# Kernel optimization log

Hardware: AMD Instinct MI355X
Metric: run time of the kernel (lower is better)

## Reference

```python
import jax, jax.numpy as jnp
import numpy as np

E = 23   # unique experts
K = 3    # active experts per token

def setup_inputs() -> dict:
    key = jax.random.key(0)
    ks = jax.random.split(key, 11)
    d, h, B, N = 1024, 768, 16, 196
    s = 0.02  # init scale so sigmoid gate is non-saturated
    return {
        "x":      jax.random.normal(ks[0], (B, N, d), jnp.float32),
        "gate_w": jax.random.normal(ks[1], (d, E), jnp.float32) * s,
        "gate_b": jnp.zeros((E,), jnp.float32),
        "w1":     jax.random.normal(ks[2], (E, d, h), jnp.float32) * s,
        "b1":     jnp.zeros((E, h), jnp.float32),
        "w2":     jax.random.normal(ks[3], (E, h, d), jnp.float32) * s,
        "b2":     jnp.zeros((E, d), jnp.float32),
        "ws1":    jax.random.normal(ks[4], (d, h), jnp.float32) * s,
        "bs1":    jnp.zeros((h,), jnp.float32),
        "ws2":    jax.random.normal(ks[5], (h, d), jnp.float32) * s,
        "bs2":    jnp.zeros((d,), jnp.float32),
    }

def reference(x, gate_w, gate_b, w1, b1, w2, b2, ws1, bs1, ws2, bs2):
    o_shape = x.shape
    xt = x.reshape(-1, o_shape[-1])            # [T, d]
    T = xt.shape[0]

    # gating: sigmoid gate, top-3 (the 'bias' buffer in the source is zeros)
    gw = jax.nn.sigmoid(xt @ gate_w + gate_b)  # [T, E]
    top_vals, top_idx = jax.lax.top_k(gw, K)   # [T, K]
    tw = top_vals / top_vals.sum(-1, keepdims=True)

    # dense combine weights: tw scattered to [T, E] (0 for unselected experts)
    w_dense = jnp.zeros_like(gw).at[jnp.arange(T)[:, None], top_idx].add(tw)

    # expert MLPs (dense-masked equivalent of the grouped dispatch)
    hh = jax.nn.gelu(jnp.einsum('td,edh->teh', xt, w1) + b1, approximate=False)
    eo = jnp.einsum('teh,ehd->ted', hh, w2) + b2          # [T, E, d]

    # shared expert
    shared = jax.nn.gelu(xt @ ws1 + bs1, approximate=False) @ ws2 + bs2

    out = shared + jnp.einsum('ted,te->td', eo, w_dense)  # [T, d]

    # aux load-balancing loss
    gwn = gw / gw.sum(-1, keepdims=True)
    P = gwn.mean(0)                                       # [E]
    counts = jnp.zeros((E,), gw.dtype).at[top_idx.reshape(-1)].add(1.0)
    Fv = E * counts / (K * T)
    aux = (P * Fv).sum()

    return out.reshape(o_shape), aux
```

## Files before the change

### kernel.cpp

```cpp
#include <hip/hip_runtime.h>
#include <hip/hip_bf16.h>

#define T_TOK 3136
#define DDIM  1024
#define HDIM  768
#define NEXP  23
#define TOPK  3
#define MTILE 128
#define NTILE 128
#define KTILE 32
#define LDSP  40
#define MAX_TILES_PER_E 25
#define MAX_SLOTS 16384
#define GATE_BLOCKS 1568
#define NBLK_T 13

typedef __attribute__((ext_vector_type(8))) short  short8;
typedef __attribute__((ext_vector_type(4))) short  short4v;
typedef __attribute__((ext_vector_type(2))) short  short2v;
typedef __attribute__((ext_vector_type(4))) float  floatx4;

__device__ __forceinline__ short f2b(float f) {
    union { float f; unsigned u; } v; v.f = f;
    unsigned r = v.u + 0x7FFFu + ((v.u >> 16) & 1u);
    return (short)(r >> 16);
}
__device__ __forceinline__ float b2f(short s) {
    union { unsigned u; float f; } v; v.u = ((unsigned)(unsigned short)s) << 16; return v.f;
}
__device__ __forceinline__ float gelu_exact(float v) {
    return 0.5f * v * (1.0f + erff(v * 0.70710678118654752f));
}

__global__ __launch_bounds__(256) void gwt_kernel(const float* __restrict__ gw, float* __restrict__ gwT) {
    __shared__ float tile[32][33];
    const int kt = blockIdx.x;
    const int tx = threadIdx.x & 31, ty = threadIdx.x >> 5;
    #pragma unroll
    for (int i = 0; i < 4; i++) {
        int k = ty + i * 8;
        tile[k][tx] = (tx < NEXP) ? gw[(size_t)(kt * 32 + k) * NEXP + tx] : 0.f;
    }
    __syncthreads();
    #pragma unroll
    for (int i = 0; i < 4; i++) {
        int e = ty + i * 8;
        if (e < 24) gwT[(size_t)e * DDIM + kt * 32 + tx] = tile[tx][e];
    }
}

__global__ __launch_bounds__(256) void prep_w_kernel(
    const float* __restrict__ w1, const float* __restrict__ ws1,
    const float* __restrict__ w2, const float* __restrict__ ws2,
    short* __restrict__ w1t, short* __restrict__ ws1t,
    short* __restrict__ w2t, short* __restrict__ ws2t)
{
    const int z = blockIdx.z;
    const float* src; short* dst; int SK, SN;
    if (z < NEXP + 1) {
        src = (z < NEXP) ? w1 + (size_t)z * DDIM * HDIM : ws1;
        dst = (z < NEXP) ? w1t + (size_t)z * DDIM * HDIM : ws1t;
        SK = DDIM; SN = HDIM;
    } else {
        int e = z - (NEXP + 1);
        src = (e < NEXP) ? w2 + (size_t)e * DDIM * HDIM : ws2;
        dst = (e < NEXP) ? w2t + (size_t)e * DDIM * HDIM : ws2t;
        SK = HDIM; SN = DDIM;
    }
    const int nt = blockIdx.x, kt = blockIdx.y;
    if (nt * 32 >= SN || kt * 64 >= SK) return;
    __shared__ float tile[64][33];
    const int tx = threadIdx.x & 31, ty = threadIdx.x >> 5;
    #pragma unroll
    for (int i = 0; i < 8; i++)
        tile[ty + i * 8][tx] = src[(size_t)(kt * 64 + ty + i * 8) * SN + nt * 32 + tx];
    __syncthreads();
    #pragma unroll
    for (int i = 0; i < 4; i++) {
        int n = ty + i * 8;
        short2v sv = { f2b(tile[2 * tx][n]), f2b(tile[2 * tx + 1][n]) };
        *(short2v*)&dst[(size_t)(nt * 32 + n) * SK + kt * 64 + 2 * tx] = sv;
    }
}

__global__ __launch_bounds__(256) void xcvt_kernel(const float* __restrict__ x, short* __restrict__ xb) {
    int i = blockIdx.x * 256 + threadIdx.x;
    float4 v = ((const float4*)x)[i];
    short4v s = { f2b(v.x), f2b(v.y), f2b(v.z), f2b(v.w) };
    ((short4v*)xb)[i] = s;
}

__global__ __launch_bounds__(256) void gate_kernel(
    const float* __restrict__ x, const float* __restrict__ gwT, const float* __restrict__ gb,
    float* __restrict__ gwn, int* __restrict__ top_idx, float* __restrict__ top_w)
{
    const int tid = threadIdx.x;
    const int lane = tid & 63, wave = tid >> 6;
    const int ebase = wave * 6;
    __shared__ float sg[24];

    for (int t = blockIdx.x; t < T_TOK; t += GATE_BLOCKS) {
        const float4* xr4 = (const float4*)(x + (size_t)t * DDIM);
        float4 xv[4];
        #pragma unroll
        for (int j = 0; j < 4; j++) xv[j] = xr4[j * 64 + lane];

        double a0 = 0, a1 = 0, a2 = 0, a3 = 0, a4 = 0, a5 = 0;
        #pragma unroll
        for (int j = 0; j < 4; j++) {
            const float4* gp = (const float4*)gwT + (size_t)ebase * 256 + j * 64 + lane;
            float4 g0 = gp[0 * 256], g1 = gp[1 * 256], g2 = gp[2 * 256];
            float4 g3 = gp[3 * 256], g4 = gp[4 * 256], g5 = gp[5 * 256];
            float4 xj = xv[j];
            a0 += (double)xj.x * g0.x + (double)xj.y * g0.y + (double)xj.z * g0.z + (double)xj.w * g0.w;
            a1 += (double)xj.x * g1.x + (double)xj.y * g1.y + (double)xj.z * g1.z + (double)xj.w * g1.w;
            a2 += (double)xj.x * g2.x + (double)xj.y * g2.y + (double)xj.z * g2.z + (double)xj.w * g2.w;
            a3 += (double)xj.x * g3.x + (double)xj.y * g3.y + (double)xj.z * g3.z + (double)xj.w * g3.w;
            a4 += (double)xj.x * g4.x + (double)xj.y * g4.y + (double)xj.z * g4.z + (double)xj.w * g4.w;
            a5 += (double)xj.x * g5.x + (double)xj.y * g5.y + (double)xj.z * g5.z + (double)xj.w * g5.w;
        }
        #pragma unroll
        for (int off = 32; off > 0; off >>= 1) {
            a0 += __shfl_xor(a0, off);
            a1 += __shfl_xor(a1, off);
            a2 += __shfl_xor(a2, off);
            a3 += __shfl_xor(a3, off);
            a4 += __shfl_xor(a4, off);
            a5 += __shfl_xor(a5, off);
        }

        if (lane == 0) {
            double av[6] = { a0, a1, a2, a3, a4, a5 };
            #pragma unroll
            for (int i = 0; i < 6; i++) {
                int e = ebase + i;
                if (e < NEXP) {
                    float z = (float)av[i] + gb[e];
                    sg[e] = 1.0f / (1.0f + expf(-z));
                }
            }
        }
        __syncthreads();

        if (tid < NEXP) {
            float s = 0.f;
            #pragma unroll
            for (int e = 0; e < NEXP; e++) s += sg[e];
            gwn[(size_t)t * NEXP + tid] = sg[tid] / s;
        }
        if (tid == 0) {
            float v0 = -1.f, v1 = -1.f, v2 = -1.f; int i0 = 0, i1 = 0, i2 = 0;
            for (int e = 0; e < NEXP; e++) {
                float v = sg[e];
                if (v > v0)      { v2 = v1; i2 = i1; v1 = v0; i1 = i0; v0 = v; i0 = e; }
                else if (v > v1) { v2 = v1; i2 = i1; v1 = v; i1 = e; }
                else if (v > v2) { v2 = v; i2 = e; }
            }
            float ts = v0 + v1 + v2;
            top_idx[t * 3 + 0] = i0; top_w[t * 3 + 0] = v0 / ts;
            top_idx[t * 3 + 1] = i1; top_w[t * 3 + 1] = v1 / ts;
            top_idx[t * 3 + 2] = i2; top_w[t * 3 + 2] = v2 / ts;
        }
        __syncthreads();
    }
}

__global__ __launch_bounds__(256) void hist_kernel(
    const int* __restrict__ top_idx, int* __restrict__ block_hist, int* __restrict__ counts)
{
    __shared__ int h[NEXP];
    const int b = blockIdx.x, tid = threadIdx.x;
    if (tid < NEXP) h[tid] = 0;
    __syncthreads();
    int t = b * 256 + tid;
    if (t < T_TOK) {
        atomicAdd(&h[top_idx[t * 3 + 0]], 1);
        atomicAdd(&h[top_idx[t * 3 + 1]], 1);
        atomicAdd(&h[top_idx[t * 3 + 2]], 1);
    }
    __syncthreads();
    if (tid < NEXP) {
        block_hist[b * NEXP + tid] = h[tid];
        atomicAdd(&counts[tid], h[tid]);
    }
}

__global__ __launch_bounds__(256) void offsets_kernel(
    const int* __restrict__ counts, const int* __restrict__ block_hist,
    int* __restrict__ offs, int* __restrict__ ntl, int* __restrict__ block_base,
    int* __restrict__ slot_t)
{
    __shared__ int soffs[NEXP + 1];
    if (threadIdx.x == 0) {
        int o = 0;
        for (int e = 0; e < NEXP; e++) {
            int nt = (counts[e] + MTILE - 1) / MTILE;
            ntl[e] = nt; offs[e] = o; soffs[e] = o; o += nt * MTILE;
        }
        ntl[NEXP] = (T_TOK + MTILE - 1) / MTILE;
        offs[NEXP] = o; soffs[NEXP] = o; o += ntl[NEXP] * MTILE;
        offs[NEXP + 1] = o;
    }
    __syncthreads();
    if (threadIdx.x < NEXP) {
        int e = threadIdx.x;
        int run = soffs[e];
        for (int b = 0; b < NBLK_T; b++) {
            block_base[b * NEXP + e] = run;
            run += block_hist[b * NEXP + e];
        }
    }
    for (int i = threadIdx.x; i < MAX_SLOTS; i += 256) slot_t[i] = 0;
}

__global__ __launch_bounds__(256) void scatter_kernel(
    const int* __restrict__ top_idx, const int* __restrict__ offs,
    const int* __restrict__ block_base,
    int* __restrict__ slot_t, int* __restrict__ slot_of)
{
    __shared__ int lfill[NEXP];
    const int b = blockIdx.x, tid = threadIdx.x;
    if (tid < NEXP) lfill[tid] = 0;
    __syncthreads();
    int t = b * 256 + tid;
    if (t < T_TOK) {
        #pragma unroll
        for (int k = 0; k < TOPK; k++) {
            int e = top_idx[t * 3 + k];
            int pos = atomicAdd(&lfill[e], 1);
            int s = block_base[b * NEXP + e] + pos;
            slot_t[s] = t;
            slot_of[t * 4 + k] = s;
        }
        int s = offs[NEXP] + t;
        slot_t[s] = t;
        slot_of[t * 4 + 3] = s;
    }
}

__global__ __launch_bounds__(256) void gemm1_kernel(
    const short* __restrict__ xb,
    const short* __restrict__ w1t, const float* __restrict__ b1,
    const short* __restrict__ ws1t, const float* __restrict__ bs1,
    const int* __restrict__ ntl, const int* __restrict__ offs,
    const int* __restrict__ slot_t, short* __restrict__ hh)
{
    const int e = blockIdx.z;
    if ((int)blockIdx.y >= ntl[e]) return;
    const int slot_base = offs[e] + blockIdx.y * MTILE;
    const int n0 = blockIdx.x * NTILE;
    const short* __restrict__ W  = (e < NEXP) ? (w1t + (size_t)e * DDIM * HDIM) : ws1t;
    const float* __restrict__ Bv = (e < NEXP) ? (b1 + (size_t)e * HDIM) : bs1;

    __shared__ __align__(16) short As[MTILE * LDSP];
    __shared__ __align__(16) short Bs[NTILE * LDSP];
    __shared__ int toks[MTILE];

    const int tid = threadIdx.x;
    for (int i = tid; i < MTILE; i += 256) toks[i] = slot_t[slot_base + i];

    const int lane = tid & 63, wave = tid >> 6;
    const int mbase = (wave & 1) * 64, nbase = (wave >> 1) * 64;
    const int lc = lane & 15, q = lane >> 4;
    const int sr = tid >> 2, sc = (tid & 3) * 8;

    floatx4 acc[4][4];
    #pragma unroll
    for (int m = 0; m < 4; m++)
        #pragma unroll
        for (int n = 0; n < 4; n++) acc[m][n] = (floatx4)0.f;

    __syncthreads();

    for (int k0 = 0; k0 < DDIM; k0 += KTILE) {
        #pragma unroll
        for (int pp = 0; pp < 2; pp++) {
            int row = sr + pp * 64;
            *(short8*)&As[row * LDSP + sc] =
                *(const short8*)(xb + (size_t)toks[row] * DDIM + k0 + sc);
            *(short8*)&Bs[row * LDSP + sc] =
                *(const short8*)(W + (size_t)(n0 + row) * DDIM + k0 + sc);
        }
        __syncthreads();
        short8 af[4], bf[4];
        #pragma unroll
        for (int m = 0; m < 4; m++) af[m] = *(const short8*)&As[(mbase + m * 16 + lc) * LDSP + q * 8];
        #pragma unroll
        for (int n = 0; n < 4; n++) bf[n] = *(const short8*)&Bs[(nbase + n * 16 + lc) * LDSP + q * 8];
        #pragma unroll
        for (int m = 0; m < 4; m++)
            #pragma unroll
            for (int n = 0; n < 4; n++)
                acc[m][n] = __builtin_amdgcn_mfma_f32_16x16x32_bf16(af[m], bf[n], acc[m][n], 0, 0, 0);
        __syncthreads();
    }

    #pragma unroll
    for (int n = 0; n < 4; n++) {
        const int col = n0 + nbase + n * 16 + lc;
        const float bb = Bv[col];
        #pragma unroll
        for (int m = 0; m < 4; m++) {
            const int rbase = slot_base + mbase + m * 16 + q * 4;
            #pragma unroll
            for (int r = 0; r < 4; r++) {
                float v = acc[m][n][r] + bb;
                hh[(size_t)(rbase + r) * HDIM + col] = f2b(gelu_exact(v));
            }
        }
    }
}

__global__ __launch_bounds__(256) void gemm2_kernel(
    const short* __restrict__ hh,
    const short* __restrict__ w2t, const float* __restrict__ b2,
    const short* __restrict__ ws2t, const float* __restrict__ bs2,
    const int* __restrict__ ntl, const int* __restrict__ offs,
    short* __restrict__ eo)
{
    const int e = blockIdx.z;
    if ((int)blockIdx.y >= ntl[e]) return;
    const int slot_base = offs[e] + blockIdx.y * MTILE;
    const int n0 = blockIdx.x * NTILE;
    const short* __restrict__ W  = (e < NEXP) ? (w2t + (size_t)e * HDIM * DDIM) : ws2t;
    const float* __restrict__ Bv = (e < NEXP) ? (b2 + (size_t)e * DDIM) : bs2;

    __shared__ __align__(16) short As[MTILE * LDSP];
    __shared__ __align__(16) short Bs[NTILE * LDSP];

    const int tid = threadIdx.x;
    const int lane = tid & 63, wave = tid >> 6;
    const int mbase = (wave & 1) * 64, nbase = (wave >> 1) * 64;
    const int lc = lane & 15, q = lane >> 4;
    const int sr = tid >> 2, sc = (tid & 3) * 8;

    floatx4 acc[4][4];
    #pragma unroll
    for (int m = 0; m < 4; m++)
        #pragma unroll
        for (int n = 0; n < 4; n++) acc[m][n] = (floatx4)0.f;

    for (int k0 = 0; k0 < HDIM; k0 += KTILE) {
        #pragma unroll
        for (int pp = 0; pp < 2; pp++) {
            int row = sr + pp * 64;
            *(short8*)&As[row * LDSP + sc] =
                *(const short8*)(hh + (size_t)(slot_base + row) * HDIM + k0 + sc);
            *(short8*)&Bs[row * LDSP + sc] =
                *(const short8*)(W + (size_t)(n0 + row) * HDIM + k0 + sc);
        }
        __syncthreads();
        short8 af[4], bf[4];
        #pragma unroll
        for (int m = 0; m < 4; m++) af[m] = *(const short8*)&As[(mbase + m * 16 + lc) * LDSP + q * 8];
        #pragma unroll
        for (int n = 0; n < 4; n++) bf[n] = *(const short8*)&Bs[(nbase + n * 16 + lc) * LDSP + q * 8];
        #pragma unroll
        for (int m = 0; m < 4; m++)
            #pragma unroll
            for (int n = 0; n < 4; n++)
                acc[m][n] = __builtin_amdgcn_mfma_f32_16x16x32_bf16(af[m], bf[n], acc[m][n], 0, 0, 0);
        __syncthreads();
    }

    #pragma unroll
    for (int n = 0; n < 4; n++) {
        const int col = n0 + nbase + n * 16 + lc;
        const float bb = Bv[col];
        #pragma unroll
        for (int m = 0; m < 4; m++) {
            const int rbase = slot_base + mbase + m * 16 + q * 4;
            #pragma unroll
            for (int r = 0; r < 4; r++)
                eo[(size_t)(rbase + r) * DDIM + col] = f2b(acc[m][n][r] + bb);
        }
    }
}

__global__ __launch_bounds__(256) void combine_kernel(
    const short* __restrict__ eo, const float* __restrict__ top_w,
    const int* __restrict__ slot_of, float* __restrict__ out)
{
    const int t = blockIdx.x;
    const int c = threadIdx.x * 4;
    const int s0 = slot_of[t * 4 + 0], s1 = slot_of[t * 4 + 1];
    const int s2 = slot_of[t * 4 + 2], s3 = slot_of[t * 4 + 3];
    const float w0 = top_w[t * 3 + 0], w1 = top_w[t * 3 + 1], w2 = top_w[t * 3 + 2];
    short4v a = *(const short4v*)(eo + (size_t)s0 * DDIM + c);
    short4v b = *(const short4v*)(eo + (size_t)s1 * DDIM + c);
    short4v d = *(const short4v*)(eo + (size_t)s2 * DDIM + c);
    short4v s = *(const short4v*)(eo + (size_t)s3 * DDIM + c);
    float4 o;
    o.x = b2f(s.x) + w0 * b2f(a.x) + w1 * b2f(b.x) + w2 * b2f(d.x);
    o.y = b2f(s.y) + w0 * b2f(a.y) + w1 * b2f(b.y) + w2 * b2f(d.y);
    o.z = b2f(s.z) + w0 * b2f(a.z) + w1 * b2f(b.z) + w2 * b2f(d.z);
    o.w = b2f(s.w) + w0 * b2f(a.w) + w1 * b2f(b.w) + w2 * b2f(d.w);
    *(float4*)(out + (size_t)t * DDIM + c) = o;
}

__global__ __launch_bounds__(256) void preduce_kernel(const float* __restrict__ gwn, float* __restrict__ Pf) {
    __shared__ float sP[NEXP];
    if (threadIdx.x < NEXP) sP[threadIdx.x] = 0.f;
    __syncthreads();
    int t = blockIdx.x * blockDim.x + threadIdx.x;
    if (t < T_TOK) {
        #pragma unroll
        for (int e = 0; e < NEXP; e++) atomicAdd(&sP[e], gwn[(size_t)t * NEXP + e]);
    }
    __syncthreads();
    if (threadIdx.x < NEXP) atomicAdd(&Pf[threadIdx.x], sP[threadIdx.x]);
}

__global__ void aux_kernel(const float* __restrict__ Pf, const int* __restrict__ counts,
                           float* __restrict__ out_aux) {
    if (threadIdx.x == 0 && blockIdx.x == 0) {
        float aux = 0.f;
        for (int e = 0; e < NEXP; e++) {
            float P = Pf[e] / (float)T_TOK;
            float F = (float)NEXP * (float)counts[e] / (float)(TOPK * T_TOK);
            aux += P * F;
        }
        out_aux[0] = aux;
    }
}

extern "C" void kernel_launch(void* const* d_in, const int* in_sizes, int n_in,
                              void* d_out, int out_size, void* d_ws, size_t ws_size,
                              hipStream_t stream)
{
    const float* x   = (const float*)d_in[0];
    const float* gw  = (const float*)d_in[1];
    const float* gb  = (const float*)d_in[2];
    const float* w1  = (const float*)d_in[3];
    const float* b1  = (const float*)d_in[4];
    const float* w2  = (const float*)d_in[5];
    const float* b2  = (const float*)d_in[6];
    const float* ws1 = (const float*)d_in[7];
    const float* bs1 = (const float*)d_in[8];
    const float* ws2 = (const float*)d_in[9];
    const float* bs2 = (const float*)d_in[10];
    float* out = (float*)d_out;

    char* p = (char*)d_ws;
    auto alloc = [&](size_t bytes) -> char* {
        char* r = p; p += (bytes + 255) & ~(size_t)255; return r;
    };
    float* gwn      = (float*)alloc((size_t)T_TOK * NEXP * 4);
    int*   top_idx  = (int*)  alloc((size_t)T_TOK * 3 * 4);
    float* top_w    = (float*)alloc((size_t)T_TOK * 3 * 4);
    int*   meta     = (int*)  alloc(2 * NEXP * 4);
    int*   counts   = meta;
    float* Pf       = (float*)(meta + NEXP);
    int*   offs     = (int*)  alloc((NEXP + 2) * 4);
    int*   ntl      = (int*)  alloc((NEXP + 1) * 4);
    int*   bhist    = (int*)  alloc((size_t)NBLK_T * NEXP * 4);
    int*   bbase    = (int*)  alloc((size_t)NBLK_T * NEXP * 4);
    int*   slot_t   = (int*)  alloc((size_t)MAX_SLOTS * 4);
    int*   slot_of  = (int*)  alloc((size_t)T_TOK * 4 * 4);
    float* gwT      = (float*)alloc((size_t)24 * DDIM * 4);
    short* xb       = (short*)alloc((size_t)T_TOK * DDIM * 2);
    short* w1t      = (short*)alloc((size_t)NEXP * DDIM * HDIM * 2);
    short* ws1t     = (short*)alloc((size_t)DDIM * HDIM * 2);
    short* w2t      = (short*)alloc((size_t)NEXP * DDIM * HDIM * 2);
    short* ws2t     = (short*)alloc((size_t)DDIM * HDIM * 2);
    short* hh       = (short*)alloc((size_t)MAX_SLOTS * HDIM * 2);
    short* eo       = (short*)alloc((size_t)MAX_SLOTS * DDIM * 2);

    hipMemsetAsync(meta, 0, 2 * NEXP * 4, stream);

    gwt_kernel<<<DDIM / 32, 256, 0, stream>>>(gw, gwT);
    prep_w_kernel<<<dim3(32, 16, 2 * (NEXP + 1)), 256, 0, stream>>>(
        w1, ws1, w2, ws2, w1t, ws1t, w2t, ws2t);
    xcvt_kernel<<<(T_TOK * DDIM / 4) / 256, 256, 0, stream>>>(x, xb);
    gate_kernel<<<GATE_BLOCKS, 256, 0, stream>>>(x, gwT, gb, gwn, top_idx, top_w);
    hist_kernel<<<NBLK_T, 256, 0, stream>>>(top_idx, bhist, counts);
    offsets_kernel<<<1, 256, 0, stream>>>(counts, bhist, offs, ntl, bbase, slot_t);
    scatter_kernel<<<NBLK_T, 256, 0, stream>>>(top_idx, offs, bbase, slot_t, slot_of);
    gemm1_kernel<<<dim3(HDIM / NTILE, MAX_TILES_PER_E, NEXP + 1), 256, 0, stream>>>(
        xb, w1t, b1, ws1t, bs1, ntl, offs, slot_t, hh);
    gemm2_kernel<<<dim3(DDIM / NTILE, MAX_TILES_PER_E, NEXP + 1), 256, 0, stream>>>(
        hh, w2t, b2, ws2t, bs2, ntl, offs, eo);
    combine_kernel<<<T_TOK, 256, 0, stream>>>(eo, top_w, slot_of, out);
    preduce_kernel<<<(T_TOK + 255) / 256, 256, 0, stream>>>(gwn, Pf);
    aux_kernel<<<1, 64, 0, stream>>>(Pf, counts, out + (size_t)T_TOK * DDIM);
}
```

Baseline: 440.3 us.

## Use direct global-to-LDS loads and a compact tile map for grouped GEMMs

The two grouped GEMM kernels now load A and B tiles with global_load_lds, which writes straight into unpadded LDS and skips the register round trip. The 3D grid of mostly empty blocks (25 tiles per expert) is replaced by a flat tile map built in offsets_kernel, so only real tiles do work and few blocks exit early. Dropping the LDS padding may add bank conflicts on the MFMA fragment reads. The main loop still has no double buffering.

```diff
diff --git a/kernel.cpp b/kernel.cpp
--- a/kernel.cpp
+++ b/kernel.cpp
@@ -9,8 +9,7 @@
 #define MTILE 128
 #define NTILE 128
 #define KTILE 32
-#define LDSP  40
-#define MAX_TILES_PER_E 25
+#define MAXTILES 128
 #define MAX_SLOTS 16384
 #define GATE_BLOCKS 1568
 #define NBLK_T 13
@@ -30,6 +29,11 @@
 }
 __device__ __forceinline__ float gelu_exact(float v) {
     return 0.5f * v * (1.0f + erff(v * 0.70710678118654752f));
+}
+__device__ __forceinline__ void gld16(const short* g, short* l) {
+    __builtin_amdgcn_global_load_lds(
+        (const __attribute__((address_space(1))) void*)g,
+        (__attribute__((address_space(3))) void*)l, 16, 0, 0);
 }
 
 __global__ __launch_bounds__(256) void gwt_kernel(const float* __restrict__ gw, float* __restrict__ gwT) {
@@ -188,18 +192,23 @@
 __global__ __launch_bounds__(256) void offsets_kernel(
     const int* __restrict__ counts, const int* __restrict__ block_hist,
     int* __restrict__ offs, int* __restrict__ ntl, int* __restrict__ block_base,
-    int* __restrict__ slot_t)
+    int* __restrict__ slot_t, int* __restrict__ tmap_e, int* __restrict__ tmap_b)
 {
     __shared__ int soffs[NEXP + 1];
     if (threadIdx.x == 0) {
-        int o = 0;
+        int o = 0, ti = 0;
         for (int e = 0; e < NEXP; e++) {
             int nt = (counts[e] + MTILE - 1) / MTILE;
-            ntl[e] = nt; offs[e] = o; soffs[e] = o; o += nt * MTILE;
-        }
-        ntl[NEXP] = (T_TOK + MTILE - 1) / MTILE;
-        offs[NEXP] = o; soffs[NEXP] = o; o += ntl[NEXP] * MTILE;
+            ntl[e] = nt; offs[e] = o; soffs[e] = o;
+            for (int j = 0; j < nt; j++) { tmap_e[ti] = e; tmap_b[ti] = o + j * MTILE; ti++; }
+            o += nt * MTILE;
+        }
+        int nts = (T_TOK + MTILE - 1) / MTILE;
+        ntl[NEXP] = nts; offs[NEXP] = o; soffs[NEXP] = o;
+        for (int j = 0; j < nts; j++) { tmap_e[ti] = NEXP; tmap_b[ti] = o + j * MTILE; ti++; }
+        o += nts * MTILE;
         offs[NEXP + 1] = o;
+        ntl[NEXP + 1] = ti;
     }
     __syncthreads();
     if (threadIdx.x < NEXP) {
@@ -242,18 +251,19 @@
     const short* __restrict__ xb,
     const short* __restrict__ w1t, const float* __restrict__ b1,
     const short* __restrict__ ws1t, const float* __restrict__ bs1,
-    const int* __restrict__ ntl, const int* __restrict__ offs,
+    const int* __restrict__ tmap_e, const int* __restrict__ tmap_b,
+    const int* __restrict__ ntl,
     const int* __restrict__ slot_t, short* __restrict__ hh)
 {
-    const int e = blockIdx.z;
-    if ((int)blockIdx.y >= ntl[e]) return;
-    const int slot_base = offs[e] + blockIdx.y * MTILE;
+    if ((int)blockIdx.y >= ntl[NEXP + 1]) return;
+    const int e = tmap_e[blockIdx.y];
+    const int slot_base = tmap_b[blockIdx.y];
     const int n0 = blockIdx.x * NTILE;
     const short* __restrict__ W  = (e < NEXP) ? (w1t + (size_t)e * DDIM * HDIM) : ws1t;
     const float* __restrict__ Bv = (e < NEXP) ? (b1 + (size_t)e * HDIM) : bs1;
 
-    __shared__ __align__(16) short As[MTILE * LDSP];
-    __shared__ __align__(16) short Bs[NTILE * LDSP];
+    __shared__ __align__(16) short As[MTILE * KTILE];
+    __shared__ __align__(16) short Bs[NTILE * KTILE];
     __shared__ int toks[MTILE];
 
     const int tid = threadIdx.x;
@@ -262,7 +272,19 @@
     const int lane = tid & 63, wave = tid >> 6;
     const int mbase = (wave & 1) * 64, nbase = (wave >> 1) * 64;
     const int lc = lane & 15, q = lane >> 4;
-    const int sr = tid >> 2, sc = (tid & 3) * 8;
+
+    const int srow = wave * 16 + (lane >> 2);
+    const int c8   = (lane & 3) * 8;
+
+    __syncthreads();
+    const short* gA0 = xb + (size_t)toks[srow]      * DDIM + c8;
+    const short* gA1 = xb + (size_t)toks[64 + srow] * DDIM + c8;
+    const short* gB0 = W + (size_t)(n0 + srow)      * DDIM + c8;
+    const short* gB1 = W + (size_t)(n0 + 64 + srow) * DDIM + c8;
+    short* lA0 = As + wave * 512;
+    short* lA1 = As + 2048 + wave * 512;
+    short* lB0 = Bs + wave * 512;
+    short* lB1 = Bs + 2048 + wave * 512;
 
     floatx4 acc[4][4];
     #pragma unroll
@@ -270,23 +292,17 @@
         #pragma unroll
         for (int n = 0; n < 4; n++) acc[m][n] = (floatx4)0.f;
 
-    __syncthreads();
-
     for (int k0 = 0; k0 < DDIM; k0 += KTILE) {
-        #pragma unroll
-        for (int pp = 0; pp < 2; pp++) {
-            int row = sr + pp * 64;
-            *(short8*)&As[row * LDSP + sc] =
-                *(const short8*)(xb + (size_t)toks[row] * DDIM + k0 + sc);
-            *(short8*)&Bs[row * LDSP + sc] =
-                *(const short8*)(W + (size_t)(n0 + row) * DDIM + k0 + sc);
-        }
+        gld16(gA0 + k0, lA0);
+        gld16(gA1 + k0, lA1);
+        gld16(gB0 + k0, lB0);
+        gld16(gB1 + k0, lB1);
         __syncthreads();
         short8 af[4], bf[4];
         #pragma unroll
-        for (int m = 0; m < 4; m++) af[m] = *(const short8*)&As[(mbase + m * 16 + lc) * LDSP + q * 8];
-        #pragma unroll
-        for (int n = 0; n < 4; n++) bf[n] = *(const short8*)&Bs[(nbase + n * 16 + lc) * LDSP + q * 8];
+        for (int m = 0; m < 4; m++) af[m] = *(const short8*)&As[(mbase + m * 16 + lc) * KTILE + q * 8];
+        #pragma unroll
+        for (int n = 0; n < 4; n++) bf[n] = *(const short8*)&Bs[(nbase + n * 16 + lc) * KTILE + q * 8];
         #pragma unroll
         for (int m = 0; m < 4; m++)
             #pragma unroll
@@ -315,24 +331,36 @@
     const short* __restrict__ hh,
     const short* __restrict__ w2t, const float* __restrict__ b2,
     const short* __restrict__ ws2t, const float* __restrict__ bs2,
-    const int* __restrict__ ntl, const int* __restrict__ offs,
+    const int* __restrict__ tmap_e, const int* __restrict__ tmap_b,
+    const int* __restrict__ ntl,
     short* __restrict__ eo)
 {
-    const int e = blockIdx.z;
-    if ((int)blockIdx.y >= ntl[e]) return;
-    const int slot_base = offs[e] + blockIdx.y * MTILE;
+    if ((int)blockIdx.y >= ntl[NEXP + 1]) return;
+    const int e = tmap_e[blockIdx.y];
+    const int slot_base = tmap_b[blockIdx.y];
     const int n0 = blockIdx.x * NTILE;
     const short* __restrict__ W  = (e < NEXP) ? (w2t + (size_t)e * HDIM * DDIM) : ws2t;
     const float* __restrict__ Bv = (e < NEXP) ? (b2 + (size_t)e * DDIM) : bs2;
 
-    __shared__ __align__(16) short As[MTILE * LDSP];
-    __shared__ __align__(16) short Bs[NTILE * LDSP];
+    __shared__ __align__(16) short As[MTILE * KTILE];
+    __shared__ __align__(16) short Bs[NTILE * KTILE];
 
     const int tid = threadIdx.x;
     const int lane = tid & 63, wave = tid >> 6;
     const int mbase = (wave & 1) * 64, nbase = (wave >> 1) * 64;
     const int lc = lane & 15, q = lane >> 4;
-    const int sr = tid >> 2, sc = (tid & 3) * 8;
+
+    const int srow = wave * 16 + (lane >> 2);
+    const int c8   = (lane & 3) * 8;
+
+    const short* gA0 = hh + (size_t)(slot_base + srow)      * HDIM + c8;
+    const short* gA1 = hh + (size_t)(slot_base + 64 + srow) * HDIM + c8;
+    const short* gB0 = W + (size_t)(n0 + srow)      * HDIM + c8;
+    const short* gB1 = W + (size_t)(n0 + 64 + srow) * HDIM + c8;
+    short* lA0 = As + wave * 512;
+    short* lA1 = As + 2048 + wave * 512;
+    short* lB0 = Bs + wave * 512;
+    short* lB1 = Bs + 2048 + wave * 512;
 
     floatx4 acc[4][4];
     #pragma unroll
@@ -341,20 +369,16 @@
         for (int n = 0; n < 4; n++) acc[m][n] = (floatx4)0.f;
 
     for (int k0 = 0; k0 < HDIM; k0 += KTILE) {
-        #pragma unroll
-        for (int pp = 0; pp < 2; pp++) {
-            int row = sr + pp * 64;
-            *(short8*)&As[row * LDSP + sc] =
-                *(const short8*)(hh + (size_t)(slot_base + row) * HDIM + k0 + sc);
-            *(short8*)&Bs[row * LDSP + sc] =
-                *(const short8*)(W + (size_t)(n0 + row) * HDIM + k0 + sc);
-        }
+        gld16(gA0 + k0, lA0);
+        gld16(gA1 + k0, lA1);
+        gld16(gB0 + k0, lB0);
+        gld16(gB1 + k0, lB1);
         __syncthreads();
         short8 af[4], bf[4];
         #pragma unroll
-        for (int m = 0; m < 4; m++) af[m] = *(const short8*)&As[(mbase + m * 16 + lc) * LDSP + q * 8];
-        #pragma unroll
-        for (int n = 0; n < 4; n++) bf[n] = *(const short8*)&Bs[(nbase + n * 16 + lc) * LDSP + q * 8];
+        for (int m = 0; m < 4; m++) af[m] = *(const short8*)&As[(mbase + m * 16 + lc) * KTILE + q * 8];
+        #pragma unroll
+        for (int n = 0; n < 4; n++) bf[n] = *(const short8*)&Bs[(nbase + n * 16 + lc) * KTILE + q * 8];
         #pragma unroll
         for (int m = 0; m < 4; m++)
             #pragma unroll
@@ -452,11 +476,13 @@
     int*   counts   = meta;
     float* Pf       = (float*)(meta + NEXP);
     int*   offs     = (int*)  alloc((NEXP + 2) * 4);
-    int*   ntl      = (int*)  alloc((NEXP + 1) * 4);
+    int*   ntl      = (int*)  alloc((NEXP + 2) * 4);
     int*   bhist    = (int*)  alloc((size_t)NBLK_T * NEXP * 4);
     int*   bbase    = (int*)  alloc((size_t)NBLK_T * NEXP * 4);
     int*   slot_t   = (int*)  alloc((size_t)MAX_SLOTS * 4);
     int*   slot_of  = (int*)  alloc((size_t)T_TOK * 4 * 4);
+    int*   tmap_e   = (int*)  alloc((size_t)MAXTILES * 4);
+    int*   tmap_b   = (int*)  alloc((size_t)MAXTILES * 4);
     float* gwT      = (float*)alloc((size_t)24 * DDIM * 4);
     short* xb       = (short*)alloc((size_t)T_TOK * DDIM * 2);
     short* w1t      = (short*)alloc((size_t)NEXP * DDIM * HDIM * 2);
@@ -474,12 +500,12 @@
     xcvt_kernel<<<(T_TOK * DDIM / 4) / 256, 256, 0, stream>>>(x, xb);
     gate_kernel<<<GATE_BLOCKS, 256, 0, stream>>>(x, gwT, gb, gwn, top_idx, top_w);
     hist_kernel<<<NBLK_T, 256, 0, stream>>>(top_idx, bhist, counts);
-    offsets_kernel<<<1, 256, 0, stream>>>(counts, bhist, offs, ntl, bbase, slot_t);
+    offsets_kernel<<<1, 256, 0, stream>>>(counts, bhist, offs, ntl, bbase, slot_t, tmap_e, tmap_b);
     scatter_kernel<<<NBLK_T, 256, 0, stream>>>(top_idx, offs, bbase, slot_t, slot_of);
-    gemm1_kernel<<<dim3(HDIM / NTILE, MAX_TILES_PER_E, NEXP + 1), 256, 0, stream>>>(
-        xb, w1t, b1, ws1t, bs1, ntl, offs, slot_t, hh);
-    gemm2_kernel<<<dim3(DDIM / NTILE, MAX_TILES_PER_E, NEXP + 1), 256, 0, stream>>>(
-        hh, w2t, b2, ws2t, bs2, ntl, offs, eo);
+    gemm1_kernel<<<dim3(HDIM / NTILE, MAXTILES), 256, 0, stream>>>(
+        xb, w1t, b1, ws1t, bs1, tmap_e, tmap_b, ntl, slot_t, hh);
+    gemm2_kernel<<<dim3(DDIM / NTILE, MAXTILES), 256, 0, stream>>>(
+        hh, w2t, b2, ws2t, bs2, tmap_e, tmap_b, ntl, eo);
     combine_kernel<<<T_TOK, 256, 0, stream>>>(eo, top_w, slot_of, out);
     preduce_kernel<<<(T_TOK + 255) / 256, 256, 0, stream>>>(gwn, Pf);
     aux_kernel<<<1, 64, 0, stream>>>(Pf, counts, out + (size_t)T_TOK * DDIM);
```

New measurement: 420.0 us. 1.05x faster.
